# Kernel tuning notes

Measured on AMD Instinct MI355X. Metric: run time of the kernel, lower is better.

## Reference

```python
import jax, jax.numpy as jnp
import numpy as np

NH = 8        # num_heads
KS = 64       # key_size
C_IN = 256
C_OUT = 3 * NH * KS   # 1536
GROUPS = 3 * NH       # 24
EPS = 1e-5
H = W = 64


def setup_inputs() -> dict:
    key = jax.random.key(0)
    k1, k2 = jax.random.split(key)
    x = jax.random.normal(k1, (1, C_IN, H, W), dtype=jnp.float32)
    conv_w = jax.random.normal(k2, (C_OUT, C_IN, 1, 1), dtype=jnp.float32) * 0.05
    gn_w = jnp.ones((C_OUT,), dtype=jnp.float32)
    gn_b = jnp.zeros((C_OUT,), dtype=jnp.float32)
    return {"x": x, "conv_w": conv_w, "gn_w": gn_w, "gn_b": gn_b}


def reference(x, conv_w, gn_w, gn_b):
    B, _, h, w = x.shape
    # 1x1 conv (normalize=True -> no bias): per-pixel GEMM over channels
    attn = jnp.einsum('bchw,oc->bohw', x, conv_w[:, :, 0, 0])  # [B, 1536, H, W]
    # GroupNorm: 24 groups of KS channels, normalized over (KS, H, W)
    g = attn.reshape(B, GROUPS, -1)
    mean = g.mean(axis=-1, keepdims=True)
    var = g.var(axis=-1, keepdims=True)
    g = (g - mean) * jax.lax.rsqrt(var + EPS)
    attn = g.reshape(B, C_OUT, h, w) * gn_w[None, :, None, None] + gn_b[None, :, None, None]
    # split into key, query, value (in that order, per chunk(3, dim=2))
    attn = attn.reshape(B, NH, 3 * KS, h * w)
    key_, query, value = jnp.split(attn, 3, axis=2)   # each [B, NH, KS, HW]
    # saliency = q^T @ k / sqrt(KS) -> [B, NH, HW, HW]
    saliency = jnp.einsum('bnkq,bnkl->bnql', query, key_) / jnp.sqrt(jnp.float32(KS))
    mask = jax.nn.softmax(saliency, axis=-1)
    # out = v @ mask^T -> [B, NH, KS, HW]
    out = jnp.einsum('bnkl,bnql->bnkq', value, mask)
    return out.reshape(B, NH * KS, h, w)
```

## Files before the change

kernel.cpp:

```cpp
#include <hip/hip_runtime.h>

typedef __bf16 bf16;
typedef __bf16 bf16x8 __attribute__((ext_vector_type(8)));
typedef __bf16 bf16x4 __attribute__((ext_vector_type(4)));
typedef float f32x4 __attribute__((ext_vector_type(4)));
typedef float f32x16 __attribute__((ext_vector_type(16)));


#define QF 0.18033688011112042f
#define EXPF(x) __builtin_amdgcn_exp2f(x)

union U4 { bf16x4 v; unsigned u[2]; };
union U8 { bf16x8 v; unsigned u[4]; };

__global__ void k_misc(const float* __restrict__ x, const float* __restrict__ w,
                       bf16* __restrict__ xT, bf16* __restrict__ wb, float* __restrict__ cs) {
    int b = blockIdx.x;
    if (b < 512) {
        int t = b * 256 + threadIdx.x;
        int p  = t & 4095;
        int c0 = (t >> 12) * 8;
        bf16x8 o;
#pragma unroll
        for (int j = 0; j < 8; j++) o[j] = (bf16)x[(c0 + j) * 4096 + p];
        *(bf16x8*)(xT + p * 256 + c0) = o;
    } else if (b < 896) {
        int idx = ((b - 512) * 256 + threadIdx.x) * 4;
        float4 f = *(const float4*)(w + idx);
        bf16x4 o;
        o[0] = (bf16)f.x; o[1] = (bf16)f.y; o[2] = (bf16)f.z; o[3] = (bf16)f.w;
        *(bf16x4*)(wb + idx) = o;
    } else {
#pragma unroll
        for (int i = 0; i < 12; i++) cs[i * 256 + threadIdx.x] = 0.f;
    }
}

__global__ __launch_bounds__(256) void k_conv(const bf16* __restrict__ Wb,
                                              const bf16* __restrict__ xT,
                                              bf16* __restrict__ qkvT,
                                              float* __restrict__ cs) {
    __shared__ __attribute__((aligned(16))) bf16 xs[64 * 72];
    __shared__ __attribute__((aligned(16))) bf16 ws2[64 * 72];
    int wid = threadIdx.x >> 6, lane = threadIdx.x & 63;
    int quad = lane >> 4, l15 = lane & 15;
    int g  = blockIdx.x % 24;
    int pb = (blockIdx.x / 24) * 64;
    int h = g / 3, sec = g % 3;
    int ob = g * 64;

    int srow = threadIdx.x >> 2;
    int scol = (threadIdx.x & 3) * 16;

    f32x4 acc[4];
#pragma unroll
    for (int c = 0; c < 4; c++) acc[c] = (f32x4){0.f, 0.f, 0.f, 0.f};

    bf16x8 fx0 = *(const bf16x8*)(xT + (pb + srow) * 256 + scol);
    bf16x8 fx1 = *(const bf16x8*)(xT + (pb + srow) * 256 + scol + 8);
    bf16x8 fw0 = *(const bf16x8*)(Wb + (ob + srow) * 256 + scol);
    bf16x8 fw1 = *(const bf16x8*)(Wb + (ob + srow) * 256 + scol + 8);

    for (int c4 = 0; c4 < 4; c4++) {
        __syncthreads();
        *(bf16x8*)(xs  + srow * 72 + scol)     = fx0;
        *(bf16x8*)(xs  + srow * 72 + scol + 8) = fx1;
        *(bf16x8*)(ws2 + srow * 72 + scol)     = fw0;
        *(bf16x8*)(ws2 + srow * 72 + scol + 8) = fw1;
        __syncthreads();

        if (c4 < 3) {
            int co = (c4 + 1) * 64;
            fx0 = *(const bf16x8*)(xT + (pb + srow) * 256 + co + scol);
            fx1 = *(const bf16x8*)(xT + (pb + srow) * 256 + co + scol + 8);
            fw0 = *(const bf16x8*)(Wb + (ob + srow) * 256 + co + scol);
            fw1 = *(const bf16x8*)(Wb + (ob + srow) * 256 + co + scol + 8);
        }

#pragma unroll
        for (int k2 = 0; k2 < 2; k2++) {
            bf16x8 a = *(const bf16x8*)(ws2 + (wid * 16 + l15) * 72 + k2 * 32 + quad * 8);
#pragma unroll
            for (int c = 0; c < 4; c++) {
                bf16x8 b = *(const bf16x8*)(xs + (c * 16 + l15) * 72 + k2 * 32 + quad * 8);
                acc[c] = __builtin_amdgcn_mfma_f32_16x16x32_bf16(a, b, acc[c], 0, 0, 0);
            }
        }
    }

    int ch0 = wid * 16 + quad * 4;
#pragma unroll
    for (int r = 0; r < 4; r++) {
        float sp  = acc[0][r] + acc[1][r] + acc[2][r] + acc[3][r];
        float ssp = acc[0][r] * acc[0][r] + acc[1][r] * acc[1][r]
                  + acc[2][r] * acc[2][r] + acc[3][r] * acc[3][r];
#pragma unroll
        for (int m = 1; m < 16; m <<= 1) {
            sp  += __shfl_xor(sp,  m, 64);
            ssp += __shfl_xor(ssp, m, 64);
        }
        if (l15 == 0) {
            atomicAdd(cs + (ob + ch0 + r) * 2,     sp);
            atomicAdd(cs + (ob + ch0 + r) * 2 + 1, ssp);
        }
    }

    __syncthreads();
    bf16* tile = xs;
    if (sec == 2) {
#pragma unroll
        for (int c = 0; c < 4; c++)
#pragma unroll
            for (int r = 0; r < 4; r++)
                tile[(ch0 + r) * 72 + c * 16 + l15] = (bf16)acc[c][r];
    } else {
#pragma unroll
        for (int c = 0; c < 4; c++) {
            bf16x4 o;
#pragma unroll
            for (int r = 0; r < 4; r++) o[r] = (bf16)acc[c][r];
            *(bf16x4*)(&tile[(c * 16 + l15) * 72 + ch0]) = o;
        }
    }
    __syncthreads();
    bf16* base = qkvT + h * 786432;
    int t = threadIdx.x;
    if (sec == 2) {
        bf16* V = base + 524288;
#pragma unroll
        for (int it = 0; it < 2; it++) {
            int e = it * 256 + t; int ch = e >> 3; int pxo = (e & 7) * 8;
            *(bf16x8*)(V + ch * 4096 + pb + pxo) = *(const bf16x8*)(&tile[ch * 72 + pxo]);
        }
    } else {
        bf16* dst = base + (sec == 0 ? 262144 : 0);
#pragma unroll
        for (int it = 0; it < 2; it++) {
            int e = it * 256 + t; int px = e >> 3; int cho = (e & 7) * 8;
            *(bf16x8*)(dst + (pb + px) * 64 + cho) = *(const bf16x8*)(&tile[px * 72 + cho]);
        }
    }
}

__global__ __launch_bounds__(256) void k_normqk(bf16* __restrict__ qkv,
                                                const float2* __restrict__ cs,
                                                const float* __restrict__ gnw,
                                                const float* __restrict__ gnb) {
    int h    = blockIdx.x >> 8;
    int base = (blockIdx.x & 255) * 2048;
    int isQ  = base < 262144;
    int g    = h * 3 + (isQ ? 1 : 0);

    int c = threadIdx.x & 63;
    float2 v = cs[g * 64 + c];
    float s = v.x, ss = v.y;
#pragma unroll
    for (int m = 1; m < 64; m <<= 1) { s += __shfl_xor(s, m, 64); ss += __shfl_xor(ss, m, 64); }
    const float N = 262144.0f;
    float mean = s / N;
    float inv  = rsqrtf(ss / N - mean * mean + 1e-5f);
    float f = isQ ? QF : 1.0f;

    int e = base + threadIdx.x * 8;
    int gc = h * 192 + (isQ ? 64 : 0) + (e & 63);
    bf16* p = qkv + h * 786432 + e;
    bf16x8 vv = *(bf16x8*)p;
    bf16x8 o;
#pragma unroll
    for (int j = 0; j < 8; j++) {
        float gw = gnw[gc + j];
        float a = inv * gw * f;
        float b = (gnb[gc + j] - mean * inv * gw) * f;
        o[j] = (bf16)(a * (float)vv[j] + b);
    }
    *(bf16x8*)p = o;
}

#define PF_BLOCK(S, PFA, PFB)                                                   \
    {                                                                           \
        float p0 = EXPF(S[0]),  p1 = EXPF(S[1]),  p2 = EXPF(S[2]),  p3 = EXPF(S[3]);   \
        float p4 = EXPF(S[4]),  p5 = EXPF(S[5]),  p6 = EXPF(S[6]),  p7 = EXPF(S[7]);   \
        float p8 = EXPF(S[8]),  p9 = EXPF(S[9]),  p10 = EXPF(S[10]), p11 = EXPF(S[11]); \
        float p12 = EXPF(S[12]), p13 = EXPF(S[13]), p14 = EXPF(S[14]), p15 = EXPF(S[15]); \
        lacc += (((p0 + p1) + (p2 + p3)) + ((p4 + p5) + (p6 + p7)))             \
              + (((p8 + p9) + (p10 + p11)) + ((p12 + p13) + (p14 + p15)));      \
        U4 lo, hi;                                                              \
        lo.v[0] = (bf16)p0;  lo.v[1] = (bf16)p1;  lo.v[2] = (bf16)p2;  lo.v[3] = (bf16)p3;  \
        hi.v[0] = (bf16)p4;  hi.v[1] = (bf16)p5;  hi.v[2] = (bf16)p6;  hi.v[3] = (bf16)p7;  \
        unsigned sa = half ? lo.u[0] : hi.u[0];                                 \
        unsigned sb = half ? lo.u[1] : hi.u[1];                                 \
        unsigned ra = (unsigned)__shfl_xor((int)sa, 32, 64);                    \
        unsigned rb = (unsigned)__shfl_xor((int)sb, 32, 64);                    \
        U8 fA;                                                                  \
        fA.u[0] = half ? ra : lo.u[0];  fA.u[1] = half ? rb : lo.u[1];          \
        fA.u[2] = half ? hi.u[0] : ra;  fA.u[3] = half ? hi.u[1] : rb;          \
        PFA = fA.v;                                                             \
        U4 lo2, hi2;                                                            \
        lo2.v[0] = (bf16)p8;  lo2.v[1] = (bf16)p9;  lo2.v[2] = (bf16)p10; lo2.v[3] = (bf16)p11; \
        hi2.v[0] = (bf16)p12; hi2.v[1] = (bf16)p13; hi2.v[2] = (bf16)p14; hi2.v[3] = (bf16)p15; \
        unsigned sc = half ? lo2.u[0] : hi2.u[0];                               \
        unsigned sd = half ? lo2.u[1] : hi2.u[1];                               \
        unsigned rc = (unsigned)__shfl_xor((int)sc, 32, 64);                    \
        unsigned rd = (unsigned)__shfl_xor((int)sd, 32, 64);                    \
        U8 fB;                                                                  \
        fB.u[0] = half ? rc : lo2.u[0];  fB.u[1] = half ? rd : lo2.u[1];        \
        fB.u[2] = half ? hi2.u[0] : rc;  fB.u[3] = half ? hi2.u[1] : rd;        \
        PFB = fB.v;                                                             \
    }

__global__ __launch_bounds__(256, 3) void k_attn(const bf16* __restrict__ qkvT,
                                                 bf16* __restrict__ Opart,
                                                 float* __restrict__ Lsum) {
    int bid   = blockIdx.x;
    int h     = bid & 7;
    int qb    = (bid >> 3) & 31;
    int split = bid >> 8;
    int wid = threadIdx.x >> 6, lane = threadIdx.x & 63;
    int l31 = lane & 31, half = lane >> 5;
    const bf16* QT = qkvT + h * 786432;
    const bf16* KT = QT + 262144;
    const bf16* V  = QT + 524288;
    int qw = qb * 128 + wid * 32;

    __shared__ __attribute__((aligned(16))) bf16 Ks[64 * 72];
    __shared__ __attribute__((aligned(16))) bf16 Vs[64 * 72];

    int r0   = threadIdx.x >> 3;
    int koff = (threadIdx.x & 7) * 8;

    bf16x8 bq[4];
#pragma unroll
    for (int ks = 0; ks < 4; ks++)
        bq[ks] = *(const bf16x8*)(QT + (qw + l31) * 64 + ks * 16 + half * 8);

    f32x16 oacc0 = (f32x16)(0.0f), oacc1 = (f32x16)(0.0f);
    float ls = 0.f;

    int t0 = (split * 64) / 3, t1 = ((split + 1) * 64) / 3;

    bf16x8 kf0, kf1, vf0, vf1;
    {
        int lb0 = t0 * 64;
        kf0 = *(const bf16x8*)(KT + (lb0 + r0) * 64 + koff);
        kf1 = *(const bf16x8*)(KT + (lb0 + r0 + 32) * 64 + koff);
        vf0 = *(const bf16x8*)(V + r0 * 4096 + lb0 + koff);
        vf1 = *(const bf16x8*)(V + (r0 + 32) * 4096 + lb0 + koff);
    }

    for (int lt = t0; lt < t1; lt++) {
        __syncthreads();
        *(bf16x8*)(Ks + r0 * 72 + koff)        = kf0;
        *(bf16x8*)(Ks + (r0 + 32) * 72 + koff) = kf1;
        *(bf16x8*)(Vs + r0 * 72 + koff)        = vf0;
        *(bf16x8*)(Vs + (r0 + 32) * 72 + koff) = vf1;
        __syncthreads();

        if (lt + 1 < t1) {
            int nb = (lt + 1) * 64;
            kf0 = *(const bf16x8*)(KT + (nb + r0) * 64 + koff);
            kf1 = *(const bf16x8*)(KT + (nb + r0 + 32) * 64 + koff);
            vf0 = *(const bf16x8*)(V + r0 * 4096 + nb + koff);
            vf1 = *(const bf16x8*)(V + (r0 + 32) * 4096 + nb + koff);
        }

        f32x16 s0 = (f32x16)(0.0f), s1 = (f32x16)(0.0f);
#pragma unroll
        for (int ks = 0; ks < 4; ks++) {
            s0 = __builtin_amdgcn_mfma_f32_32x32x16_bf16(
                *(const bf16x8*)(Ks + l31 * 72 + ks * 16 + half * 8), bq[ks], s0, 0, 0, 0);
            s1 = __builtin_amdgcn_mfma_f32_32x32x16_bf16(
                *(const bf16x8*)(Ks + (32 + l31) * 72 + ks * 16 + half * 8), bq[ks], s1, 0, 0, 0);
        }

        float lacc = ls;
        bf16x8 pf0, pf1, pf2, pf3;
        PF_BLOCK(s0, pf0, pf1);
        PF_BLOCK(s1, pf2, pf3);
        ls = lacc;

        oacc0 = __builtin_amdgcn_mfma_f32_32x32x16_bf16(
            *(const bf16x8*)(Vs + l31 * 72 +  0 + half * 8), pf0, oacc0, 0, 0, 0);
        oacc1 = __builtin_amdgcn_mfma_f32_32x32x16_bf16(
            *(const bf16x8*)(Vs + (32 + l31) * 72 +  0 + half * 8), pf0, oacc1, 0, 0, 0);
        oacc0 = __builtin_amdgcn_mfma_f32_32x32x16_bf16(
            *(const bf16x8*)(Vs + l31 * 72 + 16 + half * 8), pf1, oacc0, 0, 0, 0);
        oacc1 = __builtin_amdgcn_mfma_f32_32x32x16_bf16(
            *(const bf16x8*)(Vs + (32 + l31) * 72 + 16 + half * 8), pf1, oacc1, 0, 0, 0);
        oacc0 = __builtin_amdgcn_mfma_f32_32x32x16_bf16(
            *(const bf16x8*)(Vs + l31 * 72 + 32 + half * 8), pf2, oacc0, 0, 0, 0);
        oacc1 = __builtin_amdgcn_mfma_f32_32x32x16_bf16(
            *(const bf16x8*)(Vs + (32 + l31) * 72 + 32 + half * 8), pf2, oacc1, 0, 0, 0);
        oacc0 = __builtin_amdgcn_mfma_f32_32x32x16_bf16(
            *(const bf16x8*)(Vs + l31 * 72 + 48 + half * 8), pf3, oacc0, 0, 0, 0);
        oacc1 = __builtin_amdgcn_mfma_f32_32x32x16_bf16(
            *(const bf16x8*)(Vs + (32 + l31) * 72 + 48 + half * 8), pf3, oacc1, 0, 0, 0);
    }

    ls += __shfl_xor(ls, 32, 64);
    if (half == 0)
        Lsum[split * 32768 + h * 4096 + qw + l31] = ls;

    bf16* Ob = Opart + split * 2097152;
#pragma unroll
    for (int r = 0; r < 16; r++) {
        int kd = (r & 3) + 8 * (r >> 2) + 4 * half;
        Ob[(h * 64 + kd) * 4096 + qw + l31]        = (bf16)oacc0[r];
        Ob[(h * 64 + 32 + kd) * 4096 + qw + l31]   = (bf16)oacc1[r];
    }
}

__global__ void k_final(const bf16* __restrict__ Opart, const float* __restrict__ Lsum,
                        const float2* __restrict__ cs, const float* __restrict__ gnw,
                        const float* __restrict__ gnb, float* __restrict__ out) {
    int gid = blockIdx.x * 256 + threadIdx.x;
    int row = gid >> 9;
    int c8  = (gid & 511) << 3;
    int h   = row >> 6;

    int g = h * 3 + 2;
    int c = threadIdx.x & 63;
    float2 v = cs[g * 64 + c];
    float s = v.x, ss = v.y;
#pragma unroll
    for (int m = 1; m < 64; m <<= 1) { s += __shfl_xor(s, m, 64); ss += __shfl_xor(ss, m, 64); }
    const float N = 262144.0f;
    float mean = s / N;
    float inv  = rsqrtf(ss / N - mean * mean + 1e-5f);
    int gi = h * 192 + 128 + (row & 63);
    float gw = gnw[gi];
    float va = inv * gw;
    float vb = gnb[gi] - mean * inv * gw;

    float o[8] = {0, 0, 0, 0, 0, 0, 0, 0};
    float l[8] = {0, 0, 0, 0, 0, 0, 0, 0};
#pragma unroll
    for (int sp = 0; sp < 3; sp++) {
        bf16x8 vv = *(const bf16x8*)(Opart + sp * 2097152 + row * 4096 + c8);
        const float* L = Lsum + sp * 32768 + h * 4096 + c8;
        float4 l0 = *(const float4*)L;
        float4 l1 = *(const float4*)(L + 4);
#pragma unroll
        for (int j = 0; j < 8; j++) o[j] += (float)vv[j];
        l[0] += l0.x; l[1] += l0.y; l[2] += l0.z; l[3] += l0.w;
        l[4] += l1.x; l[5] += l1.y; l[6] += l1.z; l[7] += l1.w;
    }
    float4 r0, r1;
    r0.x = va * o[0] / l[0] + vb; r0.y = va * o[1] / l[1] + vb;
    r0.z = va * o[2] / l[2] + vb; r0.w = va * o[3] / l[3] + vb;
    r1.x = va * o[4] / l[4] + vb; r1.y = va * o[5] / l[5] + vb;
    r1.z = va * o[6] / l[6] + vb; r1.w = va * o[7] / l[7] + vb;
    *(float4*)(out + row * 4096 + c8)     = r0;
    *(float4*)(out + row * 4096 + c8 + 4) = r1;
}

extern "C" void kernel_launch(void* const* d_in, const int* in_sizes, int n_in,
                              void* d_out, int out_size, void* d_ws, size_t ws_size,
                              hipStream_t stream) {
    const float* x      = (const float*)d_in[0];
    const float* conv_w = (const float*)d_in[1];
    const float* gn_w   = (const float*)d_in[2];
    const float* gn_b   = (const float*)d_in[3];
    float* out = (float*)d_out;
    char* ws = (char*)d_ws;

    bf16*   qkvT  = (bf16*) (ws);
    bf16*   Opart = (bf16*) (ws + 12582912);
    bf16*   Wb    = (bf16*) (ws + 12582912);
    bf16*   xT    = (bf16*) (ws + 13369344);
    float*  Lsum  = (float*)(ws + 25165824);
    float*  cs    = (float*)(ws + 25559040);

    hipLaunchKernelGGL(k_misc,   dim3(897),  dim3(256), 0, stream, x, conv_w, xT, Wb, cs);
    hipLaunchKernelGGL(k_conv,   dim3(1536), dim3(256), 0, stream, Wb, xT, qkvT, cs);
    hipLaunchKernelGGL(k_normqk, dim3(2048), dim3(256), 0, stream, qkvT, (const float2*)cs, gn_w, gn_b);
    hipLaunchKernelGGL(k_attn,   dim3(768),  dim3(256), 0, stream, qkvT, Opart, Lsum);
    hipLaunchKernelGGL(k_final,  dim3(1024), dim3(256), 0, stream, Opart, Lsum, (const float2*)cs, gn_w, gn_b, out);
}
```

Before: 141.5 us.

## Fuse GroupNorm of Q and K into attention kernel, drop normqk pass

```diff
diff --git a/kernel.cpp b/kernel.cpp
--- a/kernel.cpp
+++ b/kernel.cpp
@@ -14,7 +14,7 @@
 union U8 { bf16x8 v; unsigned u[4]; };
 
 __global__ void k_misc(const float* __restrict__ x, const float* __restrict__ w,
-                       bf16* __restrict__ xT, bf16* __restrict__ wb, float* __restrict__ cs) {
+                       bf16* __restrict__ xT, bf16* __restrict__ wb) {
     int b = blockIdx.x;
     if (b < 512) {
         int t = b * 256 + threadIdx.x;
@@ -24,15 +24,12 @@
 #pragma unroll
         for (int j = 0; j < 8; j++) o[j] = (bf16)x[(c0 + j) * 4096 + p];
         *(bf16x8*)(xT + p * 256 + c0) = o;
-    } else if (b < 896) {
+    } else {
         int idx = ((b - 512) * 256 + threadIdx.x) * 4;
         float4 f = *(const float4*)(w + idx);
         bf16x4 o;
         o[0] = (bf16)f.x; o[1] = (bf16)f.y; o[2] = (bf16)f.z; o[3] = (bf16)f.w;
         *(bf16x4*)(wb + idx) = o;
-    } else {
-#pragma unroll
-        for (int i = 0; i < 12; i++) cs[i * 256 + threadIdx.x] = 0.f;
     }
 }
 
@@ -140,40 +137,6 @@
             *(bf16x8*)(dst + (pb + px) * 64 + cho) = *(const bf16x8*)(&tile[px * 72 + cho]);
         }
     }
-}
-
-__global__ __launch_bounds__(256) void k_normqk(bf16* __restrict__ qkv,
-                                                const float2* __restrict__ cs,
-                                                const float* __restrict__ gnw,
-                                                const float* __restrict__ gnb) {
-    int h    = blockIdx.x >> 8;
-    int base = (blockIdx.x & 255) * 2048;
-    int isQ  = base < 262144;
-    int g    = h * 3 + (isQ ? 1 : 0);
-
-    int c = threadIdx.x & 63;
-    float2 v = cs[g * 64 + c];
-    float s = v.x, ss = v.y;
-#pragma unroll
-    for (int m = 1; m < 64; m <<= 1) { s += __shfl_xor(s, m, 64); ss += __shfl_xor(ss, m, 64); }
-    const float N = 262144.0f;
-    float mean = s / N;
-    float inv  = rsqrtf(ss / N - mean * mean + 1e-5f);
-    float f = isQ ? QF : 1.0f;
-
-    int e = base + threadIdx.x * 8;
-    int gc = h * 192 + (isQ ? 64 : 0) + (e & 63);
-    bf16* p = qkv + h * 786432 + e;
-    bf16x8 vv = *(bf16x8*)p;
-    bf16x8 o;
-#pragma unroll
-    for (int j = 0; j < 8; j++) {
-        float gw = gnw[gc + j];
-        float a = inv * gw * f;
-        float b = (gnb[gc + j] - mean * inv * gw) * f;
-        o[j] = (bf16)(a * (float)vv[j] + b);
-    }
-    *(bf16x8*)p = o;
 }
 
 #define PF_BLOCK(S, PFA, PFB)                                                   \
@@ -209,6 +172,9 @@
     }
 
 __global__ __launch_bounds__(256, 3) void k_attn(const bf16* __restrict__ qkvT,
+                                                 const float2* __restrict__ cs,
+                                                 const float* __restrict__ gnw,
+                                                 const float* __restrict__ gnb,
                                                  bf16* __restrict__ Opart,
                                                  float* __restrict__ Lsum) {
     int bid   = blockIdx.x;
@@ -228,10 +194,41 @@
     int r0   = threadIdx.x >> 3;
     int koff = (threadIdx.x & 7) * 8;
 
+    float2 vq = cs[(h * 3 + 1) * 64 + lane];
+    float2 vk = cs[(h * 3 + 0) * 64 + lane];
+    float sq = vq.x, ssq = vq.y, sk = vk.x, ssk = vk.y;
+#pragma unroll
+    for (int m = 1; m < 64; m <<= 1) {
+        sq += __shfl_xor(sq, m, 64); ssq += __shfl_xor(ssq, m, 64);
+        sk += __shfl_xor(sk, m, 64); ssk += __shfl_xor(ssk, m, 64);
+    }
+    const float N = 262144.0f;
+    float mq = sq / N, iq = rsqrtf(ssq / N - mq * mq + 1e-5f);
+    float mk = sk / N, ik = rsqrtf(ssk / N - mk * mk + 1e-5f);
+
+    float akc[8], bkc[8];
+#pragma unroll
+    for (int j = 0; j < 8; j++) {
+        float gw = gnw[h * 192 + koff + j];
+        akc[j] = ik * gw;
+        bkc[j] = gnb[h * 192 + koff + j] - mk * akc[j];
+    }
+
     bf16x8 bq[4];
 #pragma unroll
-    for (int ks = 0; ks < 4; ks++)
-        bq[ks] = *(const bf16x8*)(QT + (qw + l31) * 64 + ks * 16 + half * 8);
+    for (int ks = 0; ks < 4; ks++) {
+        bf16x8 raw = *(const bf16x8*)(QT + (qw + l31) * 64 + ks * 16 + half * 8);
+        bf16x8 o;
+#pragma unroll
+        for (int j = 0; j < 8; j++) {
+            int ch = h * 192 + 64 + ks * 16 + half * 8 + j;
+            float gw = gnw[ch];
+            float a = iq * gw * QF;
+            float b = (gnb[ch] - mq * iq * gw) * QF;
+            o[j] = (bf16)(a * (float)raw[j] + b);
+        }
+        bq[ks] = o;
+    }
 
     f32x16 oacc0 = (f32x16)(0.0f), oacc1 = (f32x16)(0.0f);
     float ls = 0.f;
@@ -249,10 +246,18 @@
 
     for (int lt = t0; lt < t1; lt++) {
         __syncthreads();
-        *(bf16x8*)(Ks + r0 * 72 + koff)        = kf0;
-        *(bf16x8*)(Ks + (r0 + 32) * 72 + koff) = kf1;
-        *(bf16x8*)(Vs + r0 * 72 + koff)        = vf0;
-        *(bf16x8*)(Vs + (r0 + 32) * 72 + koff) = vf1;
+        {
+            bf16x8 k0, k1;
+#pragma unroll
+            for (int j = 0; j < 8; j++) {
+                k0[j] = (bf16)(akc[j] * (float)kf0[j] + bkc[j]);
+                k1[j] = (bf16)(akc[j] * (float)kf1[j] + bkc[j]);
+            }
+            *(bf16x8*)(Ks + r0 * 72 + koff)        = k0;
+            *(bf16x8*)(Ks + (r0 + 32) * 72 + koff) = k1;
+            *(bf16x8*)(Vs + r0 * 72 + koff)        = vf0;
+            *(bf16x8*)(Vs + (r0 + 32) * 72 + koff) = vf1;
+        }
         __syncthreads();
 
         if (lt + 1 < t1) {
@@ -370,9 +375,9 @@
     float*  Lsum  = (float*)(ws + 25165824);
     float*  cs    = (float*)(ws + 25559040);
 
-    hipLaunchKernelGGL(k_misc,   dim3(897),  dim3(256), 0, stream, x, conv_w, xT, Wb, cs);
-    hipLaunchKernelGGL(k_conv,   dim3(1536), dim3(256), 0, stream, Wb, xT, qkvT, cs);
-    hipLaunchKernelGGL(k_normqk, dim3(2048), dim3(256), 0, stream, qkvT, (const float2*)cs, gn_w, gn_b);
-    hipLaunchKernelGGL(k_attn,   dim3(768),  dim3(256), 0, stream, qkvT, Opart, Lsum);
-    hipLaunchKernelGGL(k_final,  dim3(1024), dim3(256), 0, stream, Opart, Lsum, (const float2*)cs, gn_w, gn_b, out);
-}
+    hipMemsetAsync(cs, 0, 12288, stream);
+    hipLaunchKernelGGL(k_misc,  dim3(896),  dim3(256), 0, stream, x, conv_w, xT, Wb);
+    hipLaunchKernelGGL(k_conv,  dim3(1536), dim3(256), 0, stream, Wb, xT, qkvT, cs);
+    hipLaunchKernelGGL(k_attn,  dim3(768),  dim3(256), 0, stream, qkvT, (const float2*)cs, gn_w, gn_b, Opart, Lsum);
+    hipLaunchKernelGGL(k_final, dim3(1024), dim3(256), 0, stream, Opart, Lsum, (const float2*)cs, gn_w, gn_b, out);
+}
```

New measurement: 140.6 us. Within noise of the previous version (-0.7%).
